# Optimization experiments

Hardware: AMD Instinct MI355X
Metric: run time of the kernel (lower is better)

The kernel has to match this reference:

```python
import jax, jax.numpy as jnp
import numpy as np

N = 100000      # num nodes
E = 1600000     # num edges (avg degree 16)
D_IN = 128
D_OUT = 128
EPS = 1e-12     # F.normalize default eps


def setup_inputs() -> dict:
    key = jax.random.key(0)
    k1, k2, k3, k4 = jax.random.split(key, 4)
    x = jax.random.normal(k1, (N, D_IN), dtype=jnp.float32)
    row = jax.random.randint(k2, (E,), 0, N, dtype=jnp.int32)
    # guarantee no self loops in the raw graph: col = (row + offset) % N, offset in [1, N)
    offset = jax.random.randint(k3, (E,), 1, N, dtype=jnp.int32)
    col = (row + offset) % N
    edge_index = jnp.stack([row, col], axis=0)
    # xavier_uniform_ for weight [in, out]
    a = np.sqrt(6.0 / (D_IN + D_OUT)).astype(np.float32)
    weight = jax.random.uniform(k4, (D_IN, D_OUT), dtype=jnp.float32, minval=-a, maxval=a)
    return {"x": x, "edge_index": edge_index, "weight": weight}


def reference(x, edge_index, weight):
    row, col = edge_index[0], edge_index[1]
    # remove_self_loops: drop edges with row == col (mask keeps shapes static)
    mask = (row != col)
    # linear transform first (as in the original forward)
    xw = jnp.matmul(x, weight)                               # [N, D_OUT]
    # scatter_mean over edges with self loops added:
    # out[i] = (sum_{j->i, j!=i} xw[j] + xw[i]) / (deg_nonself(i) + 1)
    msg = jnp.where(mask[:, None], xw[col], jnp.float32(0.0))  # [E, D_OUT]
    seg_sum = jax.ops.segment_sum(msg, row, num_segments=N) + xw
    cnt = jax.ops.segment_sum(mask.astype(xw.dtype), row, num_segments=N) + jnp.float32(1.0)
    out = seg_sum / cnt[:, None]
    # F.normalize(out, p=2, dim=-1): out / max(||out||_2, eps)
    norm = jnp.sqrt(jnp.sum(out * out, axis=-1, keepdims=True))
    out = out / jnp.maximum(norm, jnp.float32(EPS))
    return out
```

## Files before the change

kernel.cpp:

```cpp
#include <hip/hip_runtime.h>
#include <hip/hip_fp16.h>
#include <stdint.h>

#define NN 100000
#define NE 1600000
#define DD 128

#define NBKT 391
#define CAPB 4480
#define NBIN 6250
#define GCAP 512

typedef _Float16 f16x8 __attribute__((ext_vector_type(8)));
typedef float f32x4 __attribute__((ext_vector_type(4)));

__device__ __forceinline__ uint32_t hadd2u(uint32_t a, uint32_t b){
  union { uint32_t u; __half2 h; } x, y;
  x.u = a; y.u = b;
  x.h = __hadd2(x.h, y.h);
  return x.u;
}
__device__ __forceinline__ uint32_t hmul2u(uint32_t a, __half2 m){
  union { uint32_t u; __half2 h; } x; x.u = a;
  x.h = __hmul2(x.h, m);
  return x.u;
}

__global__ __launch_bounds__(256) void k_front(
    const int* __restrict__ ei, int* __restrict__ bktres, uint32_t* __restrict__ ibuf,
    const float4* __restrict__ x, uint2* __restrict__ x16,
    const float* __restrict__ w, uint16_t* __restrict__ wsw){
  int b = blockIdx.x, t = threadIdx.x;
  if (b < NBKT){
    __shared__ int sh[NBKT];
    int e0 = b*4096;
    for (int i=t; i<NBKT; i+=256) sh[i] = 0;
    __syncthreads();
    int rr[16], cc[16];
    #pragma unroll
    for (int j=0;j<16;j++){
      int e = e0 + j*256 + t;
      rr[j] = -1;
      if (e < NE){
        rr[j] = ei[e]; cc[j] = ei[NE + e];
        atomicAdd(&sh[rr[j] >> 8], 1);
      }
    }
    __syncthreads();
    for (int i=t; i<NBKT; i+=256){
      int v = sh[i];
      sh[i] = v ? atomicAdd(&bktres[i*16], v) : 0;
    }
    __syncthreads();
    #pragma unroll
    for (int j=0;j<16;j++){
      if (rr[j] >= 0){
        int bk = rr[j] >> 8;
        int p = atomicAdd(&sh[bk], 1);
        if (p < CAPB)
          ibuf[(size_t)bk*CAPB + p] = (uint32_t)(((rr[j] & 255) << 17) | cc[j]);
      }
    }
  } else if (b < 12891){
    int i = (b - NBKT)*256 + t;
    float4 v = x[i];
    union { _Float16 h[4]; uint2 u; } r;
    r.h[0] = (_Float16)v.x; r.h[1] = (_Float16)v.y;
    r.h[2] = (_Float16)v.z; r.h[3] = (_Float16)v.w;
    x16[i] = r.u;
  } else {
    int wi = (b - 12891)*256 + t;
    int j = wi & 7, l = (wi >> 3) & 63, kt = (wi >> 9) & 3, ct = wi >> 11;
    int k = kt*32 + ((l >> 4) & 3)*8 + j;
    int d = ct*16 + (l & 15);
    union { _Float16 h; uint16_t u; } cv; cv.h = (_Float16)w[k*DD + d];
    wsw[wi] = cv.u;
  }
}

__global__ __launch_bounds__(256) void k_part2(const int* __restrict__ bktres,
                                               uint32_t* __restrict__ ibuf,
                                               uint32_t* __restrict__ rowinfo){
  __shared__ uint32_t s_rec[CAPB];
  __shared__ int s_deg[256], s_off[256], s_cur[256];
  int t = threadIdx.x, lane = t & 63, wid = t >> 6;
  int b = blockIdx.x;
  int cnt = bktres[b*16]; if (cnt > CAPB) cnt = CAPB;
  size_t bb = (size_t)b*CAPB;
  s_deg[t] = 0;
  __syncthreads();
  for (int i=t; i<cnt; i+=256){
    uint32_t rec = ibuf[bb + i];
    s_rec[i] = rec;
    atomicAdd(&s_deg[rec >> 17], 1);
  }
  __syncthreads();
  if (wid == 0){
    int carry = 0;
    for (int ch=0; ch<4; ch++){
      int idx = ch*64 + lane;
      int o = s_deg[idx], v = o;
      #pragma unroll
      for (int d=1; d<64; d<<=1){ int y = __shfl_up(v, d); if (lane >= d) v += y; }
      int ex = carry + v - o;
      s_off[idx] = ex; s_cur[idx] = ex;
      carry += __shfl(v, 63);
    }
  }
  __syncthreads();
  int dgc = s_deg[t] > 255 ? 255 : s_deg[t];
  rowinfo[b*256 + t] = ((uint32_t)s_off[t] << 8) | (uint32_t)dgc;
  for (int i=t; i<cnt; i+=256){
    uint32_t rec = s_rec[i];
    int p = atomicAdd(&s_cur[rec >> 17], 1);
    ibuf[bb + p] = rec & 0x1FFFFu;
  }
}

__global__ __launch_bounds__(128, 6) void k_gather_gemm(
    const uint2* __restrict__ xp, const uint32_t* __restrict__ ibuf,
    const uint32_t* __restrict__ rowinfo, const uint16_t* __restrict__ wsw,
    float* __restrict__ out){
  __shared__ int s_col[GCAP];
  __shared__ int s_loc[16], s_deg[16];
  __shared__ uint32_t sAgg[1024];
  int t = threadIdx.x, wid = t >> 6, lane = t & 63;
  int b = blockIdx.x;
  int row0 = b << 4;
  if (t < 16){
    uint32_t info = rowinfo[row0 + t];
    s_loc[t] = (int)(info >> 8);
    s_deg[t] = (int)(info & 255u);
  }
  __syncthreads();
  int base = s_loc[0];
  int len = s_loc[15] + s_deg[15] - base; if (len > GCAP) len = GCAP;
  size_t bb = (size_t)(row0 >> 8)*CAPB + base;
  for (int i=t; i<len; i+=128) s_col[i] = (int)ibuf[bb + i];
  __syncthreads();

  int q = lane & 31, half = lane >> 5;
  for (int lr = wid; lr < 16; lr += 2){
    int n = row0 + lr;
    int dg  = s_deg[lr];
    int off = s_loc[lr] - base;
    uint2 sv = xp[(size_t)n*32 + q];
    uint32_t a01 = 0u, a23 = 0u;
    int j = 0;
    for (; j+8 <= dg; j += 8){
      int c0 = s_col[off+j+half],   c1 = s_col[off+j+2+half];
      int c2 = s_col[off+j+4+half], c3 = s_col[off+j+6+half];
      uint2 v0 = xp[(size_t)c0*32 + q]; uint2 v1 = xp[(size_t)c1*32 + q];
      uint2 v2 = xp[(size_t)c2*32 + q]; uint2 v3 = xp[(size_t)c3*32 + q];
      a01 = hadd2u(a01, v0.x); a23 = hadd2u(a23, v0.y);
      a01 = hadd2u(a01, v1.x); a23 = hadd2u(a23, v1.y);
      a01 = hadd2u(a01, v2.x); a23 = hadd2u(a23, v2.y);
      a01 = hadd2u(a01, v3.x); a23 = hadd2u(a23, v3.y);
    }
    for (; j+2 <= dg; j += 2){
      int c0 = s_col[off+j+half];
      uint2 v0 = xp[(size_t)c0*32 + q];
      a01 = hadd2u(a01, v0.x); a23 = hadd2u(a23, v0.y);
    }
    if (j < dg){
      int c0 = s_col[off+j];
      uint2 v0 = xp[(size_t)c0*32 + q];
      a01 = hadd2u(a01, half ? 0u : v0.x);
      a23 = hadd2u(a23, half ? 0u : v0.y);
    }
    a01 = hadd2u(a01, (uint32_t)__shfl_xor((int)a01, 32));
    a23 = hadd2u(a23, (uint32_t)__shfl_xor((int)a23, 32));
    __half2 inv2 = __float2half2_rn(1.0f / (float)(dg + 1));
    uint32_t r01 = hmul2u(hadd2u(a01, sv.x), inv2);
    uint32_t r23 = hmul2u(hadd2u(a23, sv.y), inv2);
    uint32_t pair = half ? r23 : r01;
    int k0 = q*4 + half*2;
    int kt = k0 >> 5, gk = (k0 >> 3) & 3, jj = k0 & 7;
    int ld = lr + (gk << 4);
    int wdx = (kt*64 + ld)*4 + (jj >> 1);
    wdx ^= (kt << 3) ^ ((gk & 1) << 2);
    sAgg[wdx] = pair;
  }
  __syncthreads();

  const f16x8* Bf = (const f16x8*)wsw;
  f16x8 a[4];
  #pragma unroll
  for (int kt=0; kt<4; kt++){
    int wb = ((kt*64 + lane)*4) ^ (kt << 3) ^ (((lane >> 4) & 1) << 2);
    a[kt] = *(const f16x8*)&sAgg[wb];
  }
  f32x4 acc[8];
  #pragma unroll
  for (int ct=0;ct<8;ct++) acc[ct] = (f32x4){0.f,0.f,0.f,0.f};
  #pragma unroll
  for (int ct=0;ct<8;ct++){
    #pragma unroll
    for (int kt=0;kt<4;kt++)
      acc[ct] = __builtin_amdgcn_mfma_f32_16x16x32_f16(a[kt], Bf[(ct*4+kt)*64 + lane], acc[ct], 0, 0, 0);
  }
  float sq[4] = {0.f,0.f,0.f,0.f};
  #pragma unroll
  for (int ct=0;ct<8;ct++){
    #pragma unroll
    for (int i=0;i<4;i++) sq[i] += acc[ct][i]*acc[ct][i];
  }
  #pragma unroll
  for (int m=1;m<16;m<<=1){
    #pragma unroll
    for (int i=0;i<4;i++) sq[i] += __shfl_xor(sq[i], m);
  }
  float sc[4];
  #pragma unroll
  for (int i=0;i<4;i++) sc[i] = 1.0f / fmaxf(sqrtf(sq[i]), 1e-12f);

  int col = lane & 15;
  int rb = row0 + ((lane >> 4) << 2);
  #pragma unroll
  for (int i=0;i<4;i++){
    int n = rb + i;
    #pragma unroll
    for (int ct=0;ct<8;ct++)
      out[(size_t)n*DD + (ct<<4) + col] = acc[ct][i]*sc[i];
  }
}

extern "C" void kernel_launch(void* const* d_in, const int* in_sizes, int n_in,
                              void* d_out, int out_size, void* d_ws, size_t ws_size,
                              hipStream_t stream){
  const float* x = (const float*)d_in[0];
  const int*  ei = (const int*)d_in[1];
  const float* w = (const float*)d_in[2];
  float* out = (float*)d_out;
  char* ws = (char*)d_ws;
  (void)in_sizes; (void)n_in; (void)out_size; (void)ws_size;

  size_t off = 0;
  uint16_t* x16 = (uint16_t*)(ws + off); off += (size_t)NN*DD*2;
  uint16_t* wsw = (uint16_t*)(ws + off); off += (size_t)DD*DD*2;
  uint32_t* ibuf = (uint32_t*)(ws + off); off += (size_t)NBKT*CAPB*4;
  int* bktres   = (int*)(ws + off); off += (size_t)NBKT*16*4;
  uint32_t* rowinfo = (uint32_t*)(ws + off); off += (size_t)NBKT*256*4;

  hipMemsetAsync(bktres, 0, (size_t)NBKT*16*4, stream);
  k_front<<<12955, 256, 0, stream>>>(ei, bktres, ibuf, (const float4*)x, (uint2*)x16, w, wsw);
  k_part2<<<NBKT, 256, 0, stream>>>(bktres, ibuf, rowinfo);
  k_gather_gemm<<<NBIN, 128, 0, stream>>>((const uint2*)x16, ibuf, rowinfo, wsw, out);
}
```

Baseline: 136.4 us.

## Assign one 16-row bin per wavefront to drop block barriers; deepen gather unroll

The gather+GEMM kernel now gives each wavefront its own 16-row bin, with private LDS slices for column indices and the aggregated tile. Row metadata moves through shuffles instead of shared memory, so all __syncthreads are replaced by a wave-local LDS wait. Previously two waves split the gather rows and then each waited at a barrier before the MFMA stage. The gather loop also gains a 16-neighbour unrolled stage, which puts more independent loads in flight. In exchange the block uses more LDS and more registers, which may lower occupancy, and each wave now gathers all 16 rows serially, so per-wave latency is longer.

```diff
diff --git a/kernel.cpp b/kernel.cpp
--- a/kernel.cpp
+++ b/kernel.cpp
@@ -117,39 +117,55 @@
   }
 }
 
-__global__ __launch_bounds__(128, 6) void k_gather_gemm(
+__global__ __launch_bounds__(256, 6) void k_gather_gemm(
     const uint2* __restrict__ xp, const uint32_t* __restrict__ ibuf,
     const uint32_t* __restrict__ rowinfo, const uint16_t* __restrict__ wsw,
     float* __restrict__ out){
-  __shared__ int s_col[GCAP];
-  __shared__ int s_loc[16], s_deg[16];
-  __shared__ uint32_t sAgg[1024];
+  __shared__ int s_col[4][GCAP];
+  __shared__ uint32_t sAgg[4][1024];
   int t = threadIdx.x, wid = t >> 6, lane = t & 63;
-  int b = blockIdx.x;
-  int row0 = b << 4;
-  if (t < 16){
-    uint32_t info = rowinfo[row0 + t];
-    s_loc[t] = (int)(info >> 8);
-    s_deg[t] = (int)(info & 255u);
-  }
-  __syncthreads();
-  int base = s_loc[0];
-  int len = s_loc[15] + s_deg[15] - base; if (len > GCAP) len = GCAP;
+  int bin = blockIdx.x*4 + wid;
+  if (bin >= NBIN) return;
+  int row0 = bin << 4;
+
+  uint32_t info = (lane < 16) ? rowinfo[row0 + lane] : 0u;
+  int loc = (int)(info >> 8), dg16 = (int)(info & 255u);
+  int base = __shfl(loc, 0);
+  int len  = __shfl(loc + dg16, 15) - base; if (len > GCAP) len = GCAP;
   size_t bb = (size_t)(row0 >> 8)*CAPB + base;
-  for (int i=t; i<len; i+=128) s_col[i] = (int)ibuf[bb + i];
-  __syncthreads();
+  int* sc = s_col[wid];
+  for (int i=lane; i<len; i+=64) sc[i] = (int)ibuf[bb + i];
 
   int q = lane & 31, half = lane >> 5;
-  for (int lr = wid; lr < 16; lr += 2){
+  uint32_t* sA = sAgg[wid];
+  for (int lr = 0; lr < 16; lr++){
     int n = row0 + lr;
-    int dg  = s_deg[lr];
-    int off = s_loc[lr] - base;
+    int dg  = __shfl(dg16, lr);
+    int off = __shfl(loc, lr) - base;
     uint2 sv = xp[(size_t)n*32 + q];
     uint32_t a01 = 0u, a23 = 0u;
     int j = 0;
+    for (; j+16 <= dg; j += 16){
+      int c0 = sc[off+j+half],    c1 = sc[off+j+2+half];
+      int c2 = sc[off+j+4+half],  c3 = sc[off+j+6+half];
+      int c4 = sc[off+j+8+half],  c5 = sc[off+j+10+half];
+      int c6 = sc[off+j+12+half], c7 = sc[off+j+14+half];
+      uint2 v0 = xp[(size_t)c0*32 + q]; uint2 v1 = xp[(size_t)c1*32 + q];
+      uint2 v2 = xp[(size_t)c2*32 + q]; uint2 v3 = xp[(size_t)c3*32 + q];
+      uint2 v4 = xp[(size_t)c4*32 + q]; uint2 v5 = xp[(size_t)c5*32 + q];
+      uint2 v6 = xp[(size_t)c6*32 + q]; uint2 v7 = xp[(size_t)c7*32 + q];
+      a01 = hadd2u(a01, v0.x); a23 = hadd2u(a23, v0.y);
+      a01 = hadd2u(a01, v1.x); a23 = hadd2u(a23, v1.y);
+      a01 = hadd2u(a01, v2.x); a23 = hadd2u(a23, v2.y);
+      a01 = hadd2u(a01, v3.x); a23 = hadd2u(a23, v3.y);
+      a01 = hadd2u(a01, v4.x); a23 = hadd2u(a23, v4.y);
+      a01 = hadd2u(a01, v5.x); a23 = hadd2u(a23, v5.y);
+      a01 = hadd2u(a01, v6.x); a23 = hadd2u(a23, v6.y);
+      a01 = hadd2u(a01, v7.x); a23 = hadd2u(a23, v7.y);
+    }
     for (; j+8 <= dg; j += 8){
-      int c0 = s_col[off+j+half],   c1 = s_col[off+j+2+half];
-      int c2 = s_col[off+j+4+half], c3 = s_col[off+j+6+half];
+      int c0 = sc[off+j+half],   c1 = sc[off+j+2+half];
+      int c2 = sc[off+j+4+half], c3 = sc[off+j+6+half];
       uint2 v0 = xp[(size_t)c0*32 + q]; uint2 v1 = xp[(size_t)c1*32 + q];
       uint2 v2 = xp[(size_t)c2*32 + q]; uint2 v3 = xp[(size_t)c3*32 + q];
       a01 = hadd2u(a01, v0.x); a23 = hadd2u(a23, v0.y);
@@ -158,12 +174,12 @@
       a01 = hadd2u(a01, v3.x); a23 = hadd2u(a23, v3.y);
     }
     for (; j+2 <= dg; j += 2){
-      int c0 = s_col[off+j+half];
+      int c0 = sc[off+j+half];
       uint2 v0 = xp[(size_t)c0*32 + q];
       a01 = hadd2u(a01, v0.x); a23 = hadd2u(a23, v0.y);
     }
     if (j < dg){
-      int c0 = s_col[off+j];
+      int c0 = sc[off+j];
       uint2 v0 = xp[(size_t)c0*32 + q];
       a01 = hadd2u(a01, half ? 0u : v0.x);
       a23 = hadd2u(a23, half ? 0u : v0.y);
@@ -179,16 +195,16 @@
     int ld = lr + (gk << 4);
     int wdx = (kt*64 + ld)*4 + (jj >> 1);
     wdx ^= (kt << 3) ^ ((gk & 1) << 2);
-    sAgg[wdx] = pair;
-  }
-  __syncthreads();
+    sA[wdx] = pair;
+  }
+  asm volatile("s_waitcnt lgkmcnt(0)" ::: "memory");
 
   const f16x8* Bf = (const f16x8*)wsw;
   f16x8 a[4];
   #pragma unroll
   for (int kt=0; kt<4; kt++){
     int wb = ((kt*64 + lane)*4) ^ (kt << 3) ^ (((lane >> 4) & 1) << 2);
-    a[kt] = *(const f16x8*)&sAgg[wb];
+    a[kt] = *(const f16x8*)&sA[wb];
   }
   f32x4 acc[8];
   #pragma unroll
@@ -210,9 +226,9 @@
     #pragma unroll
     for (int i=0;i<4;i++) sq[i] += __shfl_xor(sq[i], m);
   }
-  float sc[4];
-  #pragma unroll
-  for (int i=0;i<4;i++) sc[i] = 1.0f / fmaxf(sqrtf(sq[i]), 1e-12f);
+  float sc4[4];
+  #pragma unroll
+  for (int i=0;i<4;i++) sc4[i] = 1.0f / fmaxf(sqrtf(sq[i]), 1e-12f);
 
   int col = lane & 15;
   int rb = row0 + ((lane >> 4) << 2);
@@ -221,7 +237,7 @@
     int n = rb + i;
     #pragma unroll
     for (int ct=0;ct<8;ct++)
-      out[(size_t)n*DD + (ct<<4) + col] = acc[ct][i]*sc[i];
+      out[(size_t)n*DD + (ct<<4) + col] = acc[ct][i]*sc4[i];
   }
 }
 
@@ -245,5 +261,5 @@
   hipMemsetAsync(bktres, 0, (size_t)NBKT*16*4, stream);
   k_front<<<12955, 256, 0, stream>>>(ei, bktres, ibuf, (const float4*)x, (uint2*)x16, w, wsw);
   k_part2<<<NBKT, 256, 0, stream>>>(bktres, ibuf, rowinfo);
-  k_gather_gemm<<<NBIN, 128, 0, stream>>>((const uint2*)x16, ibuf, rowinfo, wsw, out);
-}
+  k_gather_gemm<<<(NBIN + 3)/4, 256, 0, stream>>>((const uint2*)x16, ibuf, rowinfo, wsw, out);
+}
```

Result: slower. 139.4 us (+2.2%).
